# Optimization experiments

Measured on AMD Instinct MI355X. Metric: run time of the kernel, lower is better.

Reference implementation:

```python
import jax, jax.numpy as jnp
import numpy as np

B, T, PS, DE, E, H, A, V = 32, 22, 14, 2048, 512, 512, 512, 30000

def setup_inputs() -> dict:
    key = jax.random.key(0)
    ks = jax.random.split(key, 16)
    s = 0.02
    return dict(
        features=jax.random.normal(ks[0], (B, PS, PS, DE), jnp.float32),
        captions=jax.random.randint(ks[1], (T, B), 0, V),
        caption_lengths=jax.random.randint(ks[2], (B,), 2, T + 1).at[0].set(T),
        emb=jax.random.normal(ks[3], (V, E)) * s,
        Wea=jax.random.normal(ks[4], (DE, A)) * s, bea=jnp.zeros((A,)),
        Wda=jax.random.normal(ks[5], (H, A)) * s, bda=jnp.zeros((A,)),
        Wfa=jax.random.normal(ks[6], (A, 1)) * s, bfa=jnp.zeros((1,)),
        Wih=jax.random.normal(ks[7], (4 * H, E + DE)) * s, bih=jnp.zeros((4 * H,)),
        Whh=jax.random.normal(ks[8], (4 * H, H)) * s, bhh=jnp.zeros((4 * H,)),
        Wh0=jax.random.normal(ks[9], (DE, H)) * s, bh0=jnp.zeros((H,)),
        Wc0=jax.random.normal(ks[10], (DE, H)) * s, bc0=jnp.zeros((H,)),
        Wfb=jax.random.normal(ks[11], (H, DE)) * s, bfb=jnp.zeros((DE,)),
        Wout=jax.random.normal(ks[12], (H, V)) * s, bout=jnp.zeros((V,)),
    )

def reference(features, captions, caption_lengths, emb, Wea, bea, Wda, bda,
              Wfa, bfa, Wih, bih, Whh, bhh, Wh0, bh0, Wc0, bc0, Wfb, bfb,
              Wout, bout):
    b = features.shape[0]
    enc = features.reshape(b, -1, features.shape[-1])          # [B,P,De]
    sort_ind = jnp.argsort(-caption_lengths)                   # stable, descending
    lengths = caption_lengths[sort_ind]
    enc = enc[sort_ind]
    caps = captions.T[sort_ind]                                # [B,T]
    embs = emb[caps]                                           # [B,T,E]
    mean_enc = enc.mean(axis=1)
    h0 = mean_enc @ Wh0 + bh0
    c0 = mean_enc @ Wc0 + bc0
    dec_len = lengths - 1
    Tdec = caps.shape[1] - 2                                   # = max(dec_len)-1 (setup guarantees one full-length caption)
    att1 = enc @ Wea + bea                                     # [B,P,A] precomputed (same math as per-step linear)

    def step(carry, t):
        h, c = carry
        att2 = h @ Wda + bda                                   # [B,A]
        e = (jax.nn.relu(att1 + att2[:, None, :]) @ Wfa + bfa)[..., 0]  # [B,P]
        alpha = jax.nn.softmax(e, axis=1)
        awe = jnp.einsum('bp,bpd->bd', alpha, enc)             # attention-weighted encoding
        gate = jax.nn.sigmoid(h @ Wfb + bfb)
        x = jnp.concatenate([embs[:, t, :], gate * awe], axis=1)
        gates = x @ Wih.T + bih + h @ Whh.T + bhh
        i, f, g, o = jnp.split(gates, 4, axis=1)               # torch LSTMCell gate order
        c_new = jax.nn.sigmoid(f) * c + jax.nn.sigmoid(i) * jnp.tanh(g)
        h_new = jax.nn.sigmoid(o) * jnp.tanh(c_new)
        active = (dec_len > t)[:, None]                        # shrinking-batch mask (sorted descending)
        h2 = jnp.where(active, h_new, h)
        c2 = jnp.where(active, c_new, c)
        preds = jnp.where(active, h_new @ Wout + bout, 0.0)    # dropout is identity in eval
        return (h2, c2), (preds, jnp.where(active, alpha, 0.0))

    _, (P, Al) = jax.lax.scan(step, (h0, c0), jnp.arange(Tdec))
    predictions = jnp.swapaxes(P, 0, 1)                        # [B,Tdec,V]
    alphas = jnp.swapaxes(Al, 0, 1)                            # [B,Tdec,P]
    return predictions, alphas, caps, lengths, sort_ind
```

## Files before the change

### kernel.cpp

```cpp
#include <hip/hip_runtime.h>
#include <cstdint>
#include <cstddef>

static constexpr int NB  = 32;
static constexpr int NT  = 22;
static constexpr int NP  = 196;
static constexpr int NDE = 2048;
static constexpr int NE  = 512;
static constexpr int NH  = 512;
static constexpr int NA  = 512;
static constexpr int NV  = 30000;
static constexpr int NTD = 20;
static constexpr int NKX = 3072;

static constexpr size_t OUT_PRED  = 0;
static constexpr size_t OUT_ALPHA = (size_t)NB*NTD*NV;
static constexpr size_t OUT_CAPS  = OUT_ALPHA + (size_t)NB*NTD*NP;
static constexpr size_t OUT_LEN   = OUT_CAPS + (size_t)NB*NT;
static constexpr size_t OUT_SIDX  = OUT_LEN + NB;

static constexpr size_t WS_H     = 768;
static constexpr size_t WS_C     = 17152;
static constexpr size_t WS_ATT2F = 33536;
static constexpr size_t WS_GATEF = 49920;
static constexpr size_t WS_XCATB = 121728;
static constexpr size_t WS_ATT1B = 170880;
static constexpr size_t WS_ENCB  = 1776512;
static constexpr size_t WS_W2B   = 8199040;
static constexpr size_t WS_WDAT  = 11344768;
static constexpr size_t WS_WEAT  = 11475840;
static constexpr size_t WS_WOUTT = 12000128;
static constexpr size_t WS_WFBT  = 19680128;
static constexpr size_t WS_MEANB = 20204416;
static constexpr size_t WS_WH0T  = 20237184;
static constexpr size_t WS_WC0T  = 20761472;
static constexpr size_t WS_HIST  = 21285760;

typedef __attribute__((ext_vector_type(8))) short bf16x8;
typedef __attribute__((ext_vector_type(4))) float f32x4;
#define MFMA16(a,b,c) __builtin_amdgcn_mfma_f32_16x16x32_bf16(a,b,c,0,0,0)

__device__ __forceinline__ float bf2f(unsigned short u) {
    return __uint_as_float(((unsigned)u) << 16);
}
__device__ __forceinline__ unsigned short f2bf(float f) {
    unsigned u = __float_as_uint(f);
    u += 0x7FFF + ((u >> 16) & 1);
    return (unsigned short)(u >> 16);
}
__device__ __forceinline__ float sigm(float x) { return 1.f / (1.f + expf(-x)); }


__global__ void k_sort(const int* __restrict__ cap, const int* __restrict__ clen,
                       float* __restrict__ out, int* __restrict__ wsi) {
    __shared__ int slen[NB], ssid[NB];
    int i = threadIdx.x;
    if (i < NB) slen[i] = clen[i];
    __syncthreads();
    if (i < NB) {
        int li = slen[i], r = 0;
        for (int j = 0; j < NB; j++) {
            int lj = slen[j];
            if (lj > li || (lj == li && j < i)) r++;
        }
        ssid[r] = i;
    }
    __syncthreads();
    if (i < NB) {
        int src = ssid[i];
        wsi[i] = src;
        int L = slen[src];
        wsi[NB + i] = L - 1;
        out[OUT_LEN + i]  = (float)L;
        out[OUT_SIDX + i] = (float)src;
        for (int tt = 0; tt < NT; tt++) {
            int tok = cap[tt * NB + src];
            wsi[2 * NB + i * NT + tt] = tok;
            out[OUT_CAPS + i * NT + tt] = (float)tok;
        }
    }
}

__global__ void k_prep(const float* __restrict__ feat, const int* __restrict__ wsi,
                       unsigned short* __restrict__ encb,
                       unsigned short* __restrict__ meanb) {
    int g = blockIdx.x * 256 + threadIdx.x;
    int b = g >> 11, d = g & 2047;
    const float* src = feat + (size_t)wsi[b] * (NP * NDE) + d;
    unsigned short* dst = encb + (size_t)b * (NP * NDE) + d;
    float s = 0.f;
    for (int p = 0; p < NP; p++) {
        float v = src[(size_t)p * NDE];
        s += v;
        dst[(size_t)p * NDE] = f2bf(v);
    }
    float m = s * (1.0f / 196.0f);
    meanb[(size_t)b * NDE + d] = f2bf(m);
}

__global__ __launch_bounds__(256) void k_h0c0m(const unsigned short* __restrict__ meanb,
        const unsigned short* __restrict__ WH0T, const unsigned short* __restrict__ WC0T,
        const float* __restrict__ bh0, const float* __restrict__ bc0,
        float* __restrict__ h, float* __restrict__ c, unsigned short* __restrict__ xcatb) {
    int tid = threadIdx.x;
    int w = tid >> 6, lane = tid & 63, ln = lane & 15, quad = lane >> 4;
    int which = blockIdx.x >> 3;
    int n = (blockIdx.x & 7) * 64 + w * 16 + ln;
    const unsigned short* WT = which ? WC0T : WH0T;
    f32x4 acc0 = {0.f, 0.f, 0.f, 0.f}, acc1 = {0.f, 0.f, 0.f, 0.f};
    for (int k0 = 0; k0 < NDE; k0 += 32) {
        bf16x8 bfr = *(const bf16x8*)(WT + (size_t)n * NDE + k0 + quad * 8);
        bf16x8 a0 = *(const bf16x8*)(meanb + (size_t)ln * NDE + k0 + quad * 8);
        bf16x8 a1 = *(const bf16x8*)(meanb + (size_t)(16 + ln) * NDE + k0 + quad * 8);
        acc0 = MFMA16(a0, bfr, acc0);
        acc1 = MFMA16(a1, bfr, acc1);
    }
    float bias = which ? bc0[n] : bh0[n];
    #pragma unroll
    for (int r = 0; r < 4; r++) {
        int b0r = quad * 4 + r;
        float v0 = acc0[r] + bias, v1 = acc1[r] + bias;
        if (which) {
            c[(size_t)b0r * NH + n] = v0;
            c[(size_t)(16 + b0r) * NH + n] = v1;
        } else {
            h[(size_t)b0r * NH + n] = v0;
            h[(size_t)(16 + b0r) * NH + n] = v1;
            xcatb[(size_t)b0r * NKX + 2560 + n] = f2bf(v0);
            xcatb[(size_t)(16 + b0r) * NKX + 2560 + n] = f2bf(v1);
        }
    }
}

__global__ void k_w2b(const float* __restrict__ Wih, const float* __restrict__ Whh,
                      unsigned short* __restrict__ W2b) {
    int k = blockIdx.x * 256 + threadIdx.x;
    int n = blockIdx.y;
    float v = (k < 2560) ? Wih[(size_t)n * 2560 + k]
                         : Whh[(size_t)n * 512 + (k - 2560)];
    W2b[(size_t)n * NKX + k] = f2bf(v);
}

__global__ void k_trbf(const float* __restrict__ src, unsigned short* __restrict__ dst,
                       int R, int C) {
    __shared__ float s[32][33];
    int c0 = blockIdx.x * 32, r0 = blockIdx.y * 32;
    int tx = threadIdx.x & 31, ty = threadIdx.x >> 5;
    #pragma unroll
    for (int i = 0; i < 4; i++) {
        int rr = ty * 4 + i;
        int cc = c0 + tx;
        s[rr][tx] = (cc < C) ? src[(size_t)(r0 + rr) * C + cc] : 0.f;
    }
    __syncthreads();
    #pragma unroll
    for (int i = 0; i < 4; i++) {
        int cc = ty * 4 + i;
        int cg = c0 + cc;
        if (cg < C) dst[(size_t)cg * R + r0 + tx] = f2bf(s[tx][cc]);
    }
}

__global__ __launch_bounds__(256) void k_att1(const unsigned short* __restrict__ encb,
        const unsigned short* __restrict__ WeaT, const float* __restrict__ bea,
        unsigned short* __restrict__ att1b) {
    __shared__ unsigned short As[64 * 40];
    int m0 = blockIdx.x * 64;
    int nb = blockIdx.y * 256;
    int tid = threadIdx.x;
    int w = tid >> 6, lane = tid & 63, ln = lane & 15, quad = lane >> 4;
    int nbase = nb + w * 64;
    f32x4 acc[4][4] = {};
    int sm = tid >> 2, sc = tid & 3;
    for (int k0 = 0; k0 < NDE; k0 += 32) {
        bf16x8 v = *(const bf16x8*)(encb + (size_t)(m0 + sm) * NDE + k0 + sc * 8);
        __syncthreads();
        *(bf16x8*)(&As[sm * 40 + sc * 8]) = v;
        __syncthreads();
        bf16x8 a[4], bb[4];
        #pragma unroll
        for (int i = 0; i < 4; i++)
            a[i] = *(const bf16x8*)(&As[(i * 16 + ln) * 40 + quad * 8]);
        #pragma unroll
        for (int j = 0; j < 4; j++)
            bb[j] = *(const bf16x8*)(WeaT + (size_t)(nbase + j * 16 + ln) * NDE + k0 + quad * 8);
        #pragma unroll
        for (int i = 0; i < 4; i++)
            #pragma unroll
            for (int j = 0; j < 4; j++)
                acc[i][j] = MFMA16(a[i], bb[j], acc[i][j]);
    }
    #pragma unroll
    for (int i = 0; i < 4; i++)
        #pragma unroll
        for (int j = 0; j < 4; j++) {
            int n = nbase + j * 16 + ln;
            float be = bea[n];
            #pragma unroll
            for (int r = 0; r < 4; r++) {
                int m = m0 + i * 16 + quad * 4 + r;
                att1b[(size_t)m * NA + n] = f2bf(acc[i][j][r] + be);
            }
        }
}


__global__ __launch_bounds__(256) void k_hproj(const unsigned short* __restrict__ xcatb,
        const unsigned short* __restrict__ WdaT, const unsigned short* __restrict__ WfbT,
        const float* __restrict__ bda, const float* __restrict__ bfb,
        float* __restrict__ att2f, float* __restrict__ gatef) {
    int tid = threadIdx.x;
    int w = tid >> 6, lane = tid & 63, ln = lane & 15, quad = lane >> 4;
    int n = blockIdx.x * 64 + w * 16 + ln;
    const unsigned short* wrow = (n < 512) ? (WdaT + (size_t)n * NH)
                                           : (WfbT + (size_t)(n - 512) * NH);
    f32x4 acc0 = {0.f, 0.f, 0.f, 0.f}, acc1 = {0.f, 0.f, 0.f, 0.f};
    for (int k0 = 0; k0 < NH; k0 += 32) {
        bf16x8 bfr = *(const bf16x8*)(wrow + k0 + quad * 8);
        bf16x8 a0 = *(const bf16x8*)(xcatb + (size_t)ln * NKX + 2560 + k0 + quad * 8);
        bf16x8 a1 = *(const bf16x8*)(xcatb + (size_t)(16 + ln) * NKX + 2560 + k0 + quad * 8);
        acc0 = MFMA16(a0, bfr, acc0);
        acc1 = MFMA16(a1, bfr, acc1);
    }
    float bias = (n < 512) ? bda[n] : bfb[n - 512];
    #pragma unroll
    for (int r = 0; r < 4; r++) {
        int m0 = quad * 4 + r;
        float v0 = acc0[r] + bias, v1 = acc1[r] + bias;
        if (n < 512) {
            att2f[(size_t)m0 * NA + n] = v0;
            att2f[(size_t)(16 + m0) * NA + n] = v1;
        } else {
            gatef[(size_t)m0 * NDE + (n - 512)] = v0;
            gatef[(size_t)(16 + m0) * NDE + (n - 512)] = v1;
        }
    }
}

__global__ __launch_bounds__(512) void k_attn(const float* __restrict__ emb,
        const float* __restrict__ att2f, const float* __restrict__ gatef,
        const float* __restrict__ Wfa, const float* __restrict__ bfa,
        const int* __restrict__ wsi, const unsigned short* __restrict__ att1b,
        const unsigned short* __restrict__ encb, unsigned short* __restrict__ xcatb,
        float* __restrict__ out, int t) {
    int b = blockIdx.x, dgrp = blockIdx.y;
    int tid = threadIdx.x, lane = tid & 63, wv = tid >> 6;
    __shared__ float s_att2[NA];
    __shared__ float s_e[NP];
    __shared__ float s_al[NP];
    __shared__ float sred[256];
    __shared__ float s_part[8 * 512];

    s_att2[tid] = att2f[(size_t)b * NA + tid];
    if (dgrp == 0) {
        int tok = wsi[2 * NB + b * NT + t];
        xcatb[(size_t)b * NKX + tid] = f2bf(emb[(size_t)tok * NE + tid]);
    }
    __syncthreads();

    {
        float a2r[8], wfr[8];
        #pragma unroll
        for (int u = 0; u < 8; u++) {
            a2r[u] = s_att2[lane * 8 + u];
            wfr[u] = Wfa[lane * 8 + u];
        }
        for (int p = wv; p < NP; p += 8) {
            bf16x8 a8 = *(const bf16x8*)(att1b + ((size_t)b * NP + p) * NA + lane * 8);
            float part = 0.f;
            #pragma unroll
            for (int u = 0; u < 8; u++) {
                float x = bf2f((unsigned short)a8[u]) + a2r[u];
                part = fmaf(fmaxf(x, 0.f), wfr[u], part);
            }
            #pragma unroll
            for (int off = 32; off > 0; off >>= 1) part += __shfl_down(part, off);
            if (lane == 0) s_e[p] = part + bfa[0];
        }
    }
    __syncthreads();

    if (tid < 256) sred[tid] = (tid < NP) ? s_e[tid] : -1e30f;
    __syncthreads();
    for (int s = 128; s > 0; s >>= 1) {
        if (tid < s) sred[tid] = fmaxf(sred[tid], sred[tid + s]);
        __syncthreads();
    }
    float mx = sred[0];
    __syncthreads();
    float ev = (tid < NP) ? expf(s_e[tid] - mx) : 0.f;
    if (tid < 256) sred[tid] = ev;
    __syncthreads();
    for (int s = 128; s > 0; s >>= 1) {
        if (tid < s) sred[tid] += sred[tid + s];
        __syncthreads();
    }
    float inv = 1.f / sred[0];
    if (tid < NP) {
        float a = ev * inv;
        s_al[tid] = a;
        if (dgrp == 0) {
            int active = wsi[NB + b] > t;
            out[OUT_ALPHA + ((size_t)b * NTD + t) * NP + tid] = active ? a : 0.f;
        }
    }
    __syncthreads();

    {
        float aw[8] = {0.f, 0.f, 0.f, 0.f, 0.f, 0.f, 0.f, 0.f};
        const unsigned short* base = encb + (size_t)b * (NP * NDE) + dgrp * 512 + lane * 8;
        for (int p = wv; p < NP; p += 8) {
            bf16x8 ev8 = *(const bf16x8*)(base + (size_t)p * NDE);
            float al = s_al[p];
            #pragma unroll
            for (int u = 0; u < 8; u++)
                aw[u] = fmaf(al, bf2f((unsigned short)ev8[u]), aw[u]);
        }
        #pragma unroll
        for (int u = 0; u < 8; u++)
            s_part[wv * 512 + lane * 8 + u] = aw[u];
    }
    __syncthreads();

    {
        int d = dgrp * 512 + tid;
        float s = 0.f;
        #pragma unroll
        for (int w = 0; w < 8; w++) s += s_part[w * 512 + tid];
        float g = sigm(gatef[(size_t)b * NDE + d]);
        xcatb[(size_t)b * NKX + 512 + d] = f2bf(g * s);
    }
}

__global__ __launch_bounds__(512) void k_gates(const unsigned short* __restrict__ W2b,
        unsigned short* __restrict__ xcatb, const float* __restrict__ bih,
        const float* __restrict__ bhh, const int* __restrict__ wsi,
        float* __restrict__ h, float* __restrict__ c,
        unsigned short* __restrict__ histb, int t) {
    __shared__ float red[8][2][4][64];
    int tid = threadIdx.x;
    int w = tid >> 6, lane = tid & 63, ln = lane & 15, quad = lane >> 4;
    int j0 = blockIdx.x * 4;
    int nrow = ((ln >> 2) << 9) + j0 + (ln & 3);
    f32x4 acc0 = {0.f, 0.f, 0.f, 0.f}, acc1 = {0.f, 0.f, 0.f, 0.f};
    int kb = w * 384;
    for (int ks = 0; ks < 12; ks++) {
        int k = kb + ks * 32 + quad * 8;
        bf16x8 a0 = *(const bf16x8*)(xcatb + (size_t)ln * NKX + k);
        bf16x8 a1 = *(const bf16x8*)(xcatb + (size_t)(16 + ln) * NKX + k);
        bf16x8 bq = *(const bf16x8*)(W2b + (size_t)nrow * NKX + k);
        acc0 = MFMA16(a0, bq, acc0);
        acc1 = MFMA16(a1, bq, acc1);
    }
    #pragma unroll
    for (int r = 0; r < 4; r++) {
        red[w][0][r][lane] = acc0[r];
        red[w][1][r][lane] = acc1[r];
    }
    __syncthreads();
    if (tid < 128) {
        int b = tid >> 2, j = tid & 3;
        int mh = b >> 4, row = b & 15, reg = row & 3;
        int qb = (row >> 2) << 4;
        float g4[4];
        #pragma unroll
        for (int q = 0; q < 4; q++) {
            int idx = (q << 2) | j;
            int n = q * 512 + j0 + j;
            float s = bih[n] + bhh[n];
            #pragma unroll
            for (int w2 = 0; w2 < 8; w2++) s += red[w2][mh][reg][qb | idx];
            g4[q] = s;
        }
        int jg = j0 + j;
        int active = wsi[NB + b] > t;
        float hv;
        if (active) {
            float cn = sigm(g4[1]) * c[(size_t)b * NH + jg] + sigm(g4[0]) * tanhf(g4[2]);
            hv = sigm(g4[3]) * tanhf(cn);
            c[(size_t)b * NH + jg] = cn;
            h[(size_t)b * NH + jg] = hv;
            xcatb[(size_t)b * NKX + 2560 + jg] = f2bf(hv);
        } else {
            hv = h[(size_t)b * NH + jg];
        }
        histb[((size_t)t * NB + b) * NH + jg] = f2bf(hv);
    }
}

static constexpr int HP = 520;
__global__ __launch_bounds__(256) void k_preds_all(const unsigned short* __restrict__ WoutT,
        const float* __restrict__ bout, const unsigned short* __restrict__ histb,
        const int* __restrict__ wsi, float* __restrict__ out) {
    __shared__ unsigned short s_hist[64 * HP];
    int tid = threadIdx.x;
    int w = tid >> 6, lane = tid & 63, ln = lane & 15, quad = lane >> 4;
    int n0 = blockIdx.x * 256 + w * 64;
    for (int mt = 0; mt < 5; ++mt) {
        int m0 = (blockIdx.y * 5 + mt) * 64;
        __syncthreads();
        for (int i = tid; i < 64 * 64; i += 256) {
            int r = i >> 6, cc = i & 63;
            *(bf16x8*)(&s_hist[r * HP + cc * 8]) =
                *(const bf16x8*)(histb + (size_t)(m0 + r) * NH + cc * 8);
        }
        __syncthreads();
        f32x4 acc[4][4] = {};
        for (int k0 = 0; k0 < NH; k0 += 32) {
            bf16x8 bfr[4], afr[4];
            #pragma unroll
            for (int j = 0; j < 4; j++) {
                int n = n0 + j * 16 + ln;
                int nc = (n < NV) ? n : (NV - 1);
                bfr[j] = *(const bf16x8*)(WoutT + (size_t)nc * NH + k0 + quad * 8);
            }
            #pragma unroll
            for (int i = 0; i < 4; i++)
                afr[i] = *(const bf16x8*)(&s_hist[(i * 16 + ln) * HP + k0 + quad * 8]);
            #pragma unroll
            for (int i = 0; i < 4; i++)
                #pragma unroll
                for (int j = 0; j < 4; j++)
                    acc[i][j] = MFMA16(afr[i], bfr[j], acc[i][j]);
        }
        #pragma unroll
        for (int j = 0; j < 4; j++) {
            int n = n0 + j * 16 + ln;
            if (n >= NV) continue;
            float bo = bout[n];
            #pragma unroll
            for (int i = 0; i < 4; i++) {
                #pragma unroll
                for (int r = 0; r < 4; r++) {
                    int m = m0 + i * 16 + quad * 4 + r;
                    int tt = m >> 5, b = m & 31;
                    int active = wsi[NB + b] > tt;
                    out[OUT_PRED + ((size_t)b * NTD + tt) * NV + n] =
                        active ? (acc[i][j][r] + bo) : 0.f;
                }
            }
        }
    }
}

extern "C" void kernel_launch(void* const* d_in, const int* in_sizes, int n_in,
                              void* d_out, int out_size, void* d_ws, size_t ws_size,
                              hipStream_t stream) {
    (void)in_sizes; (void)n_in; (void)out_size; (void)ws_size;
    const float* feat     = (const float*)d_in[0];
    const int*   captions = (const int*)d_in[1];
    const int*   clen     = (const int*)d_in[2];
    const float* emb      = (const float*)d_in[3];
    const float* Wea      = (const float*)d_in[4];
    const float* bea      = (const float*)d_in[5];
    const float* Wda      = (const float*)d_in[6];
    const float* bda      = (const float*)d_in[7];
    const float* Wfa      = (const float*)d_in[8];
    const float* bfa      = (const float*)d_in[9];
    const float* Wih      = (const float*)d_in[10];
    const float* bih      = (const float*)d_in[11];
    const float* Whh      = (const float*)d_in[12];
    const float* bhh      = (const float*)d_in[13];
    const float* Wh0      = (const float*)d_in[14];
    const float* bh0      = (const float*)d_in[15];
    const float* Wc0      = (const float*)d_in[16];
    const float* bc0      = (const float*)d_in[17];
    const float* Wfb      = (const float*)d_in[18];
    const float* bfb      = (const float*)d_in[19];
    const float* Wout     = (const float*)d_in[20];
    const float* bout     = (const float*)d_in[21];
    float* out = (float*)d_out;
    int*   wsi = (int*)d_ws;
    float* wsf = (float*)d_ws;

    float* W_h     = wsf + WS_H;
    float* W_c     = wsf + WS_C;
    float* W_att2f = wsf + WS_ATT2F;
    float* W_gatef = wsf + WS_GATEF;
    unsigned short* W_xcatb = (unsigned short*)(wsf + WS_XCATB);
    unsigned short* W_att1b = (unsigned short*)(wsf + WS_ATT1B);
    unsigned short* W_encb  = (unsigned short*)(wsf + WS_ENCB);
    unsigned short* W_w2b   = (unsigned short*)(wsf + WS_W2B);
    unsigned short* W_wdaT  = (unsigned short*)(wsf + WS_WDAT);
    unsigned short* W_weaT  = (unsigned short*)(wsf + WS_WEAT);
    unsigned short* W_woutT = (unsigned short*)(wsf + WS_WOUTT);
    unsigned short* W_wfbT  = (unsigned short*)(wsf + WS_WFBT);
    unsigned short* W_meanb = (unsigned short*)(wsf + WS_MEANB);
    unsigned short* W_wh0T  = (unsigned short*)(wsf + WS_WH0T);
    unsigned short* W_wc0T  = (unsigned short*)(wsf + WS_WC0T);
    unsigned short* W_hist  = (unsigned short*)(wsf + WS_HIST);

    k_sort<<<1, 64, 0, stream>>>(captions, clen, out, wsi);
    k_prep<<<256, 256, 0, stream>>>(feat, wsi, W_encb, W_meanb);
    k_trbf<<<dim3(16, 64), 256, 0, stream>>>(Wh0, W_wh0T, 2048, 512);
    k_trbf<<<dim3(16, 64), 256, 0, stream>>>(Wc0, W_wc0T, 2048, 512);
    k_h0c0m<<<16, 256, 0, stream>>>(W_meanb, W_wh0T, W_wc0T, bh0, bc0,
                                    W_h, W_c, W_xcatb);
    k_w2b<<<dim3(12, 2048), 256, 0, stream>>>(Wih, Whh, W_w2b);
    k_trbf<<<dim3(16, 16), 256, 0, stream>>>(Wda, W_wdaT, 512, 512);
    k_trbf<<<dim3(16, 64), 256, 0, stream>>>(Wea, W_weaT, 2048, 512);
    k_trbf<<<dim3(938, 16), 256, 0, stream>>>(Wout, W_woutT, 512, 30000);
    k_trbf<<<dim3(64, 16), 256, 0, stream>>>(Wfb, W_wfbT, 512, 2048);
    k_att1<<<dim3(98, 2), 256, 0, stream>>>(W_encb, W_weaT, bea, W_att1b);

    for (int t = 0; t < NTD; t++) {
        k_hproj<<<40, 256, 0, stream>>>(W_xcatb, W_wdaT, W_wfbT, bda, bfb,
                                        W_att2f, W_gatef);
        k_attn<<<dim3(32, 4), 512, 0, stream>>>(emb, W_att2f, W_gatef, Wfa, bfa,
                                                wsi, W_att1b, W_encb, W_xcatb,
                                                out, t);
        k_gates<<<128, 512, 0, stream>>>(W_w2b, W_xcatb, bih, bhh, wsi,
                                         W_h, W_c, W_hist, t);
    }
    k_preds_all<<<dim3(118, 2), 256, 0, stream>>>(W_woutT, bout, W_hist, wsi, out);
}
```

Before: 1.378 ms.

## Fuse h-projection into attention kernel and double-buffer att1 GEMM tiles

Removes the per-step k_hproj launch and computes att2 = h·Wda and the gate pre-activation h·Wfb inside k_attn, with each thread doing a scalar bf16 dot product against h held in shared memory. This removes one launch per decode step and the round trip through global att2/gate buffers. The cost is that each of the 4 d-groups per batch row recomputes the full att2 with scalar FMAs instead of MFMA, and Wda/Wfb rows are reread by every batch block. Separately, k_att1 gets a double-buffered LDS tile with a register prefetch (one sync per iteration) and a narrower N tile with twice the grid.

```diff
diff --git a/kernel.cpp b/kernel.cpp
--- a/kernel.cpp
+++ b/kernel.cpp
@@ -21,8 +21,6 @@
 
 static constexpr size_t WS_H     = 768;
 static constexpr size_t WS_C     = 17152;
-static constexpr size_t WS_ATT2F = 33536;
-static constexpr size_t WS_GATEF = 49920;
 static constexpr size_t WS_XCATB = 121728;
 static constexpr size_t WS_ATT1B = 170880;
 static constexpr size_t WS_ENCB  = 1776512;
@@ -164,36 +162,38 @@
 __global__ __launch_bounds__(256) void k_att1(const unsigned short* __restrict__ encb,
         const unsigned short* __restrict__ WeaT, const float* __restrict__ bea,
         unsigned short* __restrict__ att1b) {
-    __shared__ unsigned short As[64 * 40];
+    __shared__ unsigned short As[2][64 * 40];
     int m0 = blockIdx.x * 64;
-    int nb = blockIdx.y * 256;
+    int nb = blockIdx.y * 128;
     int tid = threadIdx.x;
     int w = tid >> 6, lane = tid & 63, ln = lane & 15, quad = lane >> 4;
-    int nbase = nb + w * 64;
-    f32x4 acc[4][4] = {};
+    int nbase = nb + w * 32;
+    f32x4 acc[4][2] = {};
     int sm = tid >> 2, sc = tid & 3;
-    for (int k0 = 0; k0 < NDE; k0 += 32) {
-        bf16x8 v = *(const bf16x8*)(encb + (size_t)(m0 + sm) * NDE + k0 + sc * 8);
+    const unsigned short* arow = encb + (size_t)(m0 + sm) * NDE + sc * 8;
+    bf16x8 v = *(const bf16x8*)(arow);
+    int p = 0;
+    for (int k0 = 0; k0 < NDE; k0 += 32, p ^= 1) {
+        *(bf16x8*)(&As[p][sm * 40 + sc * 8]) = v;
         __syncthreads();
-        *(bf16x8*)(&As[sm * 40 + sc * 8]) = v;
-        __syncthreads();
-        bf16x8 a[4], bb[4];
+        if (k0 + 32 < NDE) v = *(const bf16x8*)(arow + k0 + 32);
+        bf16x8 a[4], bb[2];
         #pragma unroll
         for (int i = 0; i < 4; i++)
-            a[i] = *(const bf16x8*)(&As[(i * 16 + ln) * 40 + quad * 8]);
-        #pragma unroll
-        for (int j = 0; j < 4; j++)
+            a[i] = *(const bf16x8*)(&As[p][(i * 16 + ln) * 40 + quad * 8]);
+        #pragma unroll
+        for (int j = 0; j < 2; j++)
             bb[j] = *(const bf16x8*)(WeaT + (size_t)(nbase + j * 16 + ln) * NDE + k0 + quad * 8);
         #pragma unroll
         for (int i = 0; i < 4; i++)
             #pragma unroll
-            for (int j = 0; j < 4; j++)
+            for (int j = 0; j < 2; j++)
                 acc[i][j] = MFMA16(a[i], bb[j], acc[i][j]);
     }
     #pragma unroll
     for (int i = 0; i < 4; i++)
         #pragma unroll
-        for (int j = 0; j < 4; j++) {
+        for (int j = 0; j < 2; j++) {
             int n = nbase + j * 16 + ln;
             float be = bea[n];
             #pragma unroll
@@ -205,56 +205,47 @@
 }
 
 
-__global__ __launch_bounds__(256) void k_hproj(const unsigned short* __restrict__ xcatb,
-        const unsigned short* __restrict__ WdaT, const unsigned short* __restrict__ WfbT,
-        const float* __restrict__ bda, const float* __restrict__ bfb,
-        float* __restrict__ att2f, float* __restrict__ gatef) {
-    int tid = threadIdx.x;
-    int w = tid >> 6, lane = tid & 63, ln = lane & 15, quad = lane >> 4;
-    int n = blockIdx.x * 64 + w * 16 + ln;
-    const unsigned short* wrow = (n < 512) ? (WdaT + (size_t)n * NH)
-                                           : (WfbT + (size_t)(n - 512) * NH);
-    f32x4 acc0 = {0.f, 0.f, 0.f, 0.f}, acc1 = {0.f, 0.f, 0.f, 0.f};
-    for (int k0 = 0; k0 < NH; k0 += 32) {
-        bf16x8 bfr = *(const bf16x8*)(wrow + k0 + quad * 8);
-        bf16x8 a0 = *(const bf16x8*)(xcatb + (size_t)ln * NKX + 2560 + k0 + quad * 8);
-        bf16x8 a1 = *(const bf16x8*)(xcatb + (size_t)(16 + ln) * NKX + 2560 + k0 + quad * 8);
-        acc0 = MFMA16(a0, bfr, acc0);
-        acc1 = MFMA16(a1, bfr, acc1);
-    }
-    float bias = (n < 512) ? bda[n] : bfb[n - 512];
-    #pragma unroll
-    for (int r = 0; r < 4; r++) {
-        int m0 = quad * 4 + r;
-        float v0 = acc0[r] + bias, v1 = acc1[r] + bias;
-        if (n < 512) {
-            att2f[(size_t)m0 * NA + n] = v0;
-            att2f[(size_t)(16 + m0) * NA + n] = v1;
-        } else {
-            gatef[(size_t)m0 * NDE + (n - 512)] = v0;
-            gatef[(size_t)(16 + m0) * NDE + (n - 512)] = v1;
-        }
-    }
-}
-
 __global__ __launch_bounds__(512) void k_attn(const float* __restrict__ emb,
-        const float* __restrict__ att2f, const float* __restrict__ gatef,
+        const unsigned short* __restrict__ WdaT, const float* __restrict__ bda,
         const float* __restrict__ Wfa, const float* __restrict__ bfa,
-        const int* __restrict__ wsi, const unsigned short* __restrict__ att1b,
-        const unsigned short* __restrict__ encb, unsigned short* __restrict__ xcatb,
-        float* __restrict__ out, int t) {
+        const int* __restrict__ wsi, const float* __restrict__ h,
+        const unsigned short* __restrict__ att1b, const unsigned short* __restrict__ encb,
+        const unsigned short* __restrict__ WfbT, const float* __restrict__ bfb,
+        unsigned short* __restrict__ xcatb, float* __restrict__ out, int t) {
     int b = blockIdx.x, dgrp = blockIdx.y;
     int tid = threadIdx.x, lane = tid & 63, wv = tid >> 6;
+    int d = dgrp * 512 + tid;
+    __shared__ float s_h[NH];
     __shared__ float s_att2[NA];
-    __shared__ float s_e[NP];
-    __shared__ float s_al[NP];
+    __shared__ float s_e[256];
+    __shared__ float s_al[256];
     __shared__ float sred[256];
     __shared__ float s_part[8 * 512];
 
-    s_att2[tid] = att2f[(size_t)b * NA + tid];
+    s_h[tid] = h[(size_t)b * NH + tid];
     if (dgrp == 0) {
         int tok = wsi[2 * NB + b * NT + t];
         xcatb[(size_t)b * NKX + tid] = f2bf(emb[(size_t)tok * NE + tid]);
+    }
+    __syncthreads();
+
+    {
+        const unsigned short* wdar = WdaT + (size_t)tid * NH;
+        float a0 = bda[tid], a1 = 0.f, a2 = 0.f, a3 = 0.f;
+        for (int k0 = 0; k0 < NH; k0 += 32) {
+            bf16x8 w0 = *(const bf16x8*)(wdar + k0);
+            bf16x8 w1 = *(const bf16x8*)(wdar + k0 + 8);
+            bf16x8 w2 = *(const bf16x8*)(wdar + k0 + 16);
+            bf16x8 w3 = *(const bf16x8*)(wdar + k0 + 24);
+            #pragma unroll
+            for (int u = 0; u < 8; u++) {
+                a0 = fmaf(s_h[k0 + u],      bf2f((unsigned short)w0[u]), a0);
+                a1 = fmaf(s_h[k0 + 8 + u],  bf2f((unsigned short)w1[u]), a1);
+                a2 = fmaf(s_h[k0 + 16 + u], bf2f((unsigned short)w2[u]), a2);
+                a3 = fmaf(s_h[k0 + 24 + u], bf2f((unsigned short)w3[u]), a3);
+            }
+        }
+        s_att2[tid] = (a0 + a1) + (a2 + a3);
     }
     __syncthreads();
 
@@ -323,12 +314,26 @@
     __syncthreads();
 
     {
-        int d = dgrp * 512 + tid;
-        float s = 0.f;
-        #pragma unroll
-        for (int w = 0; w < 8; w++) s += s_part[w * 512 + tid];
-        float g = sigm(gatef[(size_t)b * NDE + d]);
-        xcatb[(size_t)b * NKX + 512 + d] = f2bf(g * s);
+        float aw = 0.f;
+        #pragma unroll
+        for (int w2 = 0; w2 < 8; w2++) aw += s_part[w2 * 512 + tid];
+        const unsigned short* wfbr = WfbT + (size_t)d * NH;
+        float g0 = bfb[d], g1 = 0.f, g2 = 0.f, g3 = 0.f;
+        for (int k0 = 0; k0 < NH; k0 += 32) {
+            bf16x8 w0 = *(const bf16x8*)(wfbr + k0);
+            bf16x8 w1 = *(const bf16x8*)(wfbr + k0 + 8);
+            bf16x8 w2 = *(const bf16x8*)(wfbr + k0 + 16);
+            bf16x8 w3 = *(const bf16x8*)(wfbr + k0 + 24);
+            #pragma unroll
+            for (int u = 0; u < 8; u++) {
+                g0 = fmaf(s_h[k0 + u],      bf2f((unsigned short)w0[u]), g0);
+                g1 = fmaf(s_h[k0 + 8 + u],  bf2f((unsigned short)w1[u]), g1);
+                g2 = fmaf(s_h[k0 + 16 + u], bf2f((unsigned short)w2[u]), g2);
+                g3 = fmaf(s_h[k0 + 24 + u], bf2f((unsigned short)w3[u]), g3);
+            }
+        }
+        float g = (g0 + g1) + (g2 + g3);
+        xcatb[(size_t)b * NKX + 512 + d] = f2bf(sigm(g) * aw);
     }
 }
 
@@ -475,8 +480,6 @@
 
     float* W_h     = wsf + WS_H;
     float* W_c     = wsf + WS_C;
-    float* W_att2f = wsf + WS_ATT2F;
-    float* W_gatef = wsf + WS_GATEF;
     unsigned short* W_xcatb = (unsigned short*)(wsf + WS_XCATB);
     unsigned short* W_att1b = (unsigned short*)(wsf + WS_ATT1B);
     unsigned short* W_encb  = (unsigned short*)(wsf + WS_ENCB);
@@ -501,14 +504,12 @@
     k_trbf<<<dim3(16, 64), 256, 0, stream>>>(Wea, W_weaT, 2048, 512);
     k_trbf<<<dim3(938, 16), 256, 0, stream>>>(Wout, W_woutT, 512, 30000);
     k_trbf<<<dim3(64, 16), 256, 0, stream>>>(Wfb, W_wfbT, 512, 2048);
-    k_att1<<<dim3(98, 2), 256, 0, stream>>>(W_encb, W_weaT, bea, W_att1b);
+    k_att1<<<dim3(98, 4), 256, 0, stream>>>(W_encb, W_weaT, bea, W_att1b);
 
     for (int t = 0; t < NTD; t++) {
-        k_hproj<<<40, 256, 0, stream>>>(W_xcatb, W_wdaT, W_wfbT, bda, bfb,
-                                        W_att2f, W_gatef);
-        k_attn<<<dim3(32, 4), 512, 0, stream>>>(emb, W_att2f, W_gatef, Wfa, bfa,
-                                                wsi, W_att1b, W_encb, W_xcatb,
-                                                out, t);
+        k_attn<<<dim3(32, 4), 512, 0, stream>>>(emb, W_wdaT, bda, Wfa, bfa, wsi,
+                                                W_h, W_att1b, W_encb, W_wfbT, bfb,
+                                                W_xcatb, out, t);
         k_gates<<<128, 512, 0, stream>>>(W_w2b, W_xcatb, bih, bhh, wsi,
                                          W_h, W_c, W_hist, t);
     }
```

Result: slower. 1.770 ms (+28.5%).
